# Kernel tuning notes

Hardware: AMD Instinct MI355X
Metric: run time of the kernel (lower is better)

## Reference

```python
import jax, jax.numpy as jnp
import numpy as np

# Module hyperparameters (match torch init_kwargs)
D_MODEL = 512
N_HEADS = 8
WINDOW_LEN = 128
DIL_FACTOR = 64
N_DIL = 2
ATTN_SINK = True
SRC_LEN = 2048
BSZ = 2


def setup_inputs() -> dict:
    key = jax.random.key(0)
    ks = jax.random.split(key, 6)
    w_scale = 0.04  # ~ xavier_uniform scale for 512x512
    inp = {
        "x": jax.random.normal(ks[0], (SRC_LEN, BSZ, D_MODEL), jnp.float32),
        "Wq": jax.random.normal(ks[1], (D_MODEL, D_MODEL), jnp.float32) * w_scale,
        "bq": jnp.zeros((D_MODEL,), jnp.float32),
        "Wk": jax.random.normal(ks[2], (D_MODEL, D_MODEL), jnp.float32) * w_scale,
        "bk": jnp.zeros((D_MODEL,), jnp.float32),
        "Wv": jax.random.normal(ks[3], (D_MODEL, D_MODEL), jnp.float32) * w_scale,
        "bv": jnp.zeros((D_MODEL,), jnp.float32),
        "Wo": jax.random.normal(ks[4], (D_MODEL, D_MODEL), jnp.float32) * w_scale,
        "bo": jnp.zeros((D_MODEL,), jnp.float32),
        "beta": jnp.zeros((N_HEADS,), jnp.float32),
    }
    return inp


def _fast_attention(x, Wq, bq, Wk, bk, Wv, bv, Wo, bo, beta):
    s, b, dm = x.shape  # (src_len, bsz, d_model)
    h = N_HEADS
    d = dm // h
    q = x @ Wq.T + bq
    k = x @ Wk.T + bk
    v = x @ Wv.T + bv

    def split_heads(t):  # 's b (h d) -> (b h) s d'
        return t.reshape(s, b, h, d).transpose(1, 2, 0, 3).reshape(b * h, s, d)

    q, k, v = split_heads(q), split_heads(k), split_heads(v)

    # beta: per-head temperature, tiled over batch (matches torch .repeat(bsz,1,1))
    beta_e = jnp.tile(jnp.exp(beta), b)[:, None, None]  # (b*h, 1, 1)
    q = q / (jnp.sqrt(jnp.asarray(d, q.dtype)) * beta_e)

    attn_out = jnp.zeros_like(v)
    z = b * h
    for i in range(N_DIL):
        dil = DIL_FACTOR ** i
        p = (WINDOW_LEN - 1) * dil
        pad = (p % s) if (p % s) != p else 0  # static python ints
        nw = pad // dil + 1  # num windows
        # causal left-padded strided windowed view of q: (z, nw, s, d)
        qp = jnp.pad(q, ((0, 0), (pad, 0), (0, 0)))
        idx = (jnp.arange(nw) * dil)[:, None] + jnp.arange(s)[None, :]  # (nw, s)
        qi = qp[:, idx, :]
        w = jnp.einsum('zbsd,zsd->zbs', qi, k)  # (z, nw, s)
        if ATTN_SINK:
            w = jnp.concatenate([w, jnp.zeros((z, 1, s), w.dtype)], axis=1)
        w = jax.nn.softmax(w, axis=1)  # softmax over window axis (+ sink)
        if ATTN_SINK:
            w = w[:, :-1]
        k2 = jnp.einsum('zbs,zsd->zbd', w, k)  # (z, nw, d)
        v2 = jnp.einsum('zbs,zsd->zbd', w, v)
        # left-pad back to full length (zeros at front, values at end)
        k = jnp.pad(k2, ((0, 0), (s - nw, 0), (0, 0)))
        v = jnp.pad(v2, ((0, 0), (s - nw, 0), (0, 0)))
        attn_out = attn_out + v

    # '(b h) s d -> s b (h d)'
    out = attn_out.reshape(b, h, s, d).transpose(2, 0, 1, 3).reshape(s, b, dm)
    return out @ Wo.T + bo


def reference(x, Wq, bq, Wk, bk, Wv, bv, Wo, bo, beta):
    return _fast_attention(x, Wq, bq, Wk, bk, Wv, bv, Wo, bo, beta)
```

## Files before the change

kernel.cpp:

```cpp
#include <hip/hip_runtime.h>
#include <math.h>

#define S_LEN 2048
#define BSZ 2
#define DM 512
#define NH 8
#define HD 64
#define RTOT (S_LEN*BSZ)
#define T_KEEP 32
#define ROW0 ((S_LEN - T_KEEP)*BSZ)

typedef __attribute__((ext_vector_type(8))) _Float16 half8;
typedef __attribute__((ext_vector_type(4))) float floatx4;

__device__ __forceinline__ half8 pack8(float4 a, float4 b) {
    half8 h;
    h[0]=(_Float16)a.x; h[1]=(_Float16)a.y; h[2]=(_Float16)a.z; h[3]=(_Float16)a.w;
    h[4]=(_Float16)b.x; h[5]=(_Float16)b.y; h[6]=(_Float16)b.z; h[7]=(_Float16)b.w;
    return h;
}

__global__ __launch_bounds__(256, 1) void mega(
    const float* __restrict__ x,
    const float* __restrict__ Wq, const float* __restrict__ Wk,
    const float* __restrict__ bq, const float* __restrict__ bk,
    const float* __restrict__ beta, const float* __restrict__ bo,
    float* __restrict__ spart, float* __restrict__ ssump,
    float* __restrict__ qsel, float* __restrict__ out)
{
    __shared__ __align__(16) char smem[65536];

    const int tid  = threadIdx.x;
    const int w    = tid >> 6;
    const int lane = tid & 63;
    const int lrow = lane & 15;
    const int lk8  = lane >> 4;
    const int bid  = blockIdx.x;
    const int rc   = (bid & 7)*4 + (bid >> 6);
    const int h    = (bid >> 3) & 7;
    const int r0   = rc * 128;

    {
        const float4* b4 = (const float4*)bo;
        float4* o4 = (float4*)out + (size_t)bid*2016;
        const int base = bid*2016;
        #pragma unroll
        for (int i = 0; i < 8; ++i) {
            int idx = i*256 + tid;
            if (idx < 2016) o4[idx] = b4[(base + idx) & 127];
        }
    }

    const int jsub = lk8;
    const int l15  = lrow;

    #pragma unroll
    for (int i = 0; i < 8; ++i) {
        const int chunk = w*8 + i;
        const int j = chunk*4 + jsub;
        const int s = l15 ^ (j & 15);
        const float* src = (j < 64 ? Wq + (size_t)(h*HD + j)*DM
                                   : Wk + (size_t)(h*HD + j - 64)*DM) + s*8;
        float4 f0 = *(const float4*)src;
        float4 f1 = *(const float4*)(src + 4);
        *(half8*)(smem + chunk*1024 + jsub*256 + l15*16) = pack8(f0, f1);
    }

    const float* xA = x + (size_t)(r0 + w*16 + lrow)*DM + lk8*8;
    const float* xB = x + (size_t)(r0 + (w+4)*16 + lrow)*DM + lk8*8;

    half8 Aa[4], Ab[4];
    #pragma unroll
    for (int kc2 = 0; kc2 < 4; ++kc2) {
        Aa[kc2] = pack8(*(const float4*)(xA + kc2*32), *(const float4*)(xA + kc2*32 + 4));
        Ab[kc2] = pack8(*(const float4*)(xB + kc2*32), *(const float4*)(xB + kc2*32 + 4));
    }

    floatx4 acc[2][8];
    #pragma unroll
    for (int jt = 0; jt < 8; ++jt) { acc[0][jt] = (floatx4)0.f; acc[1][jt] = (floatx4)0.f; }

    __syncthreads();

    #pragma unroll
    for (int kq = 0; kq < 4; ++kq) {
        const char* buf = smem + (kq & 1)*32768;
        char* nb = smem + ((kq + 1) & 1)*32768;

        float4 WF0[8], WF1[8];
        if (kq < 3) {
            #pragma unroll
            for (int i = 0; i < 8; ++i) {
                const int j = (w*8 + i)*4 + jsub;
                const int s = l15 ^ (j & 15);
                const float* src = (j < 64 ? Wq + (size_t)(h*HD + j)*DM
                                           : Wk + (size_t)(h*HD + j - 64)*DM)
                                   + (kq+1)*128 + s*8;
                WF0[i] = *(const float4*)src;
                WF1[i] = *(const float4*)(src + 4);
            }
        }

        #pragma unroll
        for (int kc2 = 0; kc2 < 4; ++kc2) {
            #pragma unroll
            for (int jt = 0; jt < 8; ++jt) {
                const int j = jt*16 + lrow;
                const int slotp = (kc2*4 + lk8) ^ lrow;
                half8 bf = *(const half8*)(buf + j*256 + slotp*16);
                acc[0][jt] = __builtin_amdgcn_mfma_f32_16x16x32_f16(Aa[kc2], bf, acc[0][jt], 0, 0, 0);
                acc[1][jt] = __builtin_amdgcn_mfma_f32_16x16x32_f16(Ab[kc2], bf, acc[1][jt], 0, 0, 0);
            }
            if (kq < 3) {
                Aa[kc2] = pack8(*(const float4*)(xA + (kq+1)*128 + kc2*32),
                                *(const float4*)(xA + (kq+1)*128 + kc2*32 + 4));
                Ab[kc2] = pack8(*(const float4*)(xB + (kq+1)*128 + kc2*32),
                                *(const float4*)(xB + (kq+1)*128 + kc2*32 + 4));
            }
        }

        if (kq < 3) {
            #pragma unroll
            for (int i = 0; i < 8; ++i)
                *(half8*)(nb + (w*8 + i)*1024 + jsub*256 + l15*16) = pack8(WF0[i], WF1[i]);
        }
        __syncthreads();
    }

    float* s_sig = (float*)smem;
    float bqv[4], bkv[4];
    #pragma unroll
    for (int jt = 0; jt < 4; ++jt) {
        bqv[jt] = bq[h*HD + jt*16 + lrow];
        bkv[jt] = bk[h*HD + jt*16 + lrow];
    }
    const float isc = 1.0f / (8.0f * expf(beta[h]));

    #pragma unroll
    for (int t = 0; t < 2; ++t) {
        #pragma unroll
        for (int r = 0; r < 4; ++r) {
            float q[4]; float p = 0.f;
            #pragma unroll
            for (int jt = 0; jt < 4; ++jt) {
                float qv = acc[t][jt][r]   + bqv[jt];
                float kv = acc[t][jt+4][r] + bkv[jt];
                q[jt] = qv;
                p += qv * kv;
            }
            p += __shfl_xor(p, 1, 64);
            p += __shfl_xor(p, 2, 64);
            p += __shfl_xor(p, 4, 64);
            p += __shfl_xor(p, 8, 64);
            const int rowl = (w + t*4)*16 + lk8*4 + r;
            if (lrow == 0)
                s_sig[rowl] = 1.0f / (1.0f + expf(-p * isc));
            if (rowl >= 126) {
                const int b = rowl & 1;
                float* qd = &qsel[((size_t)((b*NH + h)*T_KEEP) + rc)*64];
                #pragma unroll
                for (int jt = 0; jt < 4; ++jt) qd[jt*16 + lrow] = q[jt];
            }
        }
    }
    __syncthreads();

    {
        const int b  = tid & 1;
        const int cg = tid >> 1;
        const float* px = x + (size_t)(r0 + b)*DM + cg*4;
        float a0=0.f, a1=0.f, a2=0.f, a3=0.f;
        #pragma unroll 16
        for (int si = 0; si < 64; ++si) {
            const float sg = s_sig[si*2 + b];
            const float4 xv = *(const float4*)(px + (size_t)(si*2)*DM);
            a0 += sg*xv.x; a1 += sg*xv.y; a2 += sg*xv.z; a3 += sg*xv.w;
        }
        float4 st; st.x = a0; st.y = a1; st.z = a2; st.w = a3;
        *(float4*)&spart[((size_t)(rc*2 + b)*8 + h)*512 + cg*4] = st;
    }
    if (tid < 2) {
        float s = 0.f;
        for (int i = 0; i < 64; ++i) s += s_sig[i*2 + tid];
        ssump[(rc*2 + tid)*8 + h] = s;
    }
}

__global__ __launch_bounds__(256) void kvc(
    const float* __restrict__ spart, const float* __restrict__ ssump,
    const float* __restrict__ qsel, const float* __restrict__ beta,
    const float* __restrict__ Wk, const float* __restrict__ bk,
    const float* __restrict__ Wv, const float* __restrict__ bv,
    float* __restrict__ vbar, float* __restrict__ coef)
{
    const int z  = blockIdx.x >> 1;
    const int kv = blockIdx.x & 1;
    const int b  = z >> 3;
    const int h  = z & 7;
    const int tid = threadIdx.x;

    __shared__ float s_sb[DM];
    __shared__ float s_red[64][4];
    __shared__ float s_kb[64];
    __shared__ float s_part[T_KEEP][8];
    __shared__ float s_S;

    {
        const float2* sp = (const float2*)spart;
        float ax = 0.f, ay = 0.f;
        #pragma unroll
        for (int rcc = 0; rcc < 32; ++rcc) {
            float2 v = sp[((size_t)(rcc*2 + b)*8 + h)*256 + tid];
            ax += v.x; ay += v.y;
        }
        s_sb[tid*2] = ax; s_sb[tid*2+1] = ay;
    }
    {
        float sv = 0.f;
        if (tid < 32) sv = ssump[(tid*2 + b)*8 + h];
        if (tid < 64) {
            sv += __shfl_xor(sv, 1, 64);
            sv += __shfl_xor(sv, 2, 64);
            sv += __shfl_xor(sv, 4, 64);
            sv += __shfl_xor(sv, 8, 64);
            sv += __shfl_xor(sv, 16, 64);
            if (tid == 0) s_S = sv;
        }
    }
    __syncthreads();
    const float S = s_S;

    const float* W    = kv ? Wv : Wk;
    const float* bvec = kv ? bv : bk;
    {
        const int j = tid >> 2, kp = tid & 3;
        const float* wr = &W[(size_t)(h*HD + j)*DM + kp*128];
        float a = 0.f;
        #pragma unroll
        for (int k = 0; k < 128; k += 4) {
            float4 w4 = *(const float4*)&wr[k];
            int k0 = kp*128 + k;
            a += w4.x*s_sb[k0] + w4.y*s_sb[k0+1] + w4.z*s_sb[k0+2] + w4.w*s_sb[k0+3];
        }
        s_red[j][kp] = a;
    }
    __syncthreads();
    if (tid < 64) {
        float val = s_red[tid][0]+s_red[tid][1]+s_red[tid][2]+s_red[tid][3]
                  + bvec[h*HD + tid]*S;
        if (kv) vbar[z*HD + tid] = val;
        else    s_kb[tid] = val;
    }
    if (kv) return;
    __syncthreads();
    {
        const int wi = tid >> 3, jg = tid & 7;
        const float* qrow = &qsel[((size_t)z*T_KEEP + wi)*64 + jg*8];
        float4 q1 = *(const float4*)qrow;
        float4 q2 = *(const float4*)(qrow + 4);
        const int j0 = jg*8;
        float p = q1.x*s_kb[j0]   + q1.y*s_kb[j0+1] + q1.z*s_kb[j0+2] + q1.w*s_kb[j0+3]
                + q2.x*s_kb[j0+4] + q2.y*s_kb[j0+5] + q2.z*s_kb[j0+6] + q2.w*s_kb[j0+7];
        s_part[wi][jg] = p;
    }
    __syncthreads();
    if (tid < T_KEEP) {
        float sc = 0.f;
        #pragma unroll
        for (int gg = 0; gg < 8; ++gg) sc += s_part[tid][gg];
        sc *= 1.0f / (8.0f * expf(beta[h]));
        float m = sc;
        #pragma unroll
        for (int off = 16; off > 0; off >>= 1) m = fmaxf(m, __shfl_xor(m, off, 64));
        m = fmaxf(m, 0.f);
        float e = expf(sc - m);
        float d = e;
        #pragma unroll
        for (int off = 16; off > 0; off >>= 1) d += __shfl_xor(d, off, 64);
        d += expf(-m);
        float c = e / d;
        if (tid == T_KEEP-1) c += 1.0f;
        coef[z*T_KEEP + tid] = c;
    }
}

__global__ __launch_bounds__(256) void gout(
    const float* __restrict__ coef, const float* __restrict__ vbar,
    const float* __restrict__ Wo, const float* __restrict__ bo,
    float* __restrict__ out)
{
    const int b  = blockIdx.x & 1;
    const int cc = blockIdx.x >> 1;
    const int tid = threadIdx.x;

    __shared__ float s_cf[NH][T_KEEP];
    __shared__ float s_vb[NH*HD];
    __shared__ float s_gp[16][NH][2];

    s_vb[tid]       = vbar[b*512 + tid];
    s_vb[tid + 256] = vbar[b*512 + 256 + tid];
    s_cf[tid >> 5][tid & 31] = coef[((size_t)(b*NH) + (tid >> 5))*T_KEEP + (tid & 31)];
    __syncthreads();

    {
        const int ci = tid & 15, hh = (tid >> 4) & 7, j2 = tid >> 7;
        const float* wr = &Wo[(size_t)(cc*16 + ci)*DM + hh*HD + j2*32];
        const float* vb = &s_vb[hh*HD + j2*32];
        float a = 0.f;
        #pragma unroll
        for (int j = 0; j < 32; j += 4) {
            float4 w4 = *(const float4*)&wr[j];
            a += w4.x*vb[j] + w4.y*vb[j+1] + w4.z*vb[j+2] + w4.w*vb[j+3];
        }
        s_gp[ci][hh][j2] = a;
    }
    __syncthreads();
    {
        const int ci = tid & 15;
        const float bov = bo[cc*16 + ci];
        #pragma unroll
        for (int hf = 0; hf < 2; ++hf) {
            const int wi = (tid >> 4) + hf*16;
            float v = bov;
            #pragma unroll
            for (int hh = 0; hh < NH; ++hh)
                v += s_cf[hh][wi] * (s_gp[ci][hh][0] + s_gp[ci][hh][1]);
            out[(size_t)(ROW0 + wi*2 + b)*DM + cc*16 + ci] = v;
        }
    }
}

extern "C" void kernel_launch(void* const* d_in, const int* in_sizes, int n_in,
                              void* d_out, int out_size, void* d_ws, size_t ws_size,
                              hipStream_t stream) {
    const float* x    = (const float*)d_in[0];
    const float* Wq   = (const float*)d_in[1];
    const float* bq   = (const float*)d_in[2];
    const float* Wk   = (const float*)d_in[3];
    const float* bk   = (const float*)d_in[4];
    const float* Wv   = (const float*)d_in[5];
    const float* bv   = (const float*)d_in[6];
    const float* Wo   = (const float*)d_in[7];
    const float* bo   = (const float*)d_in[8];
    const float* beta = (const float*)d_in[9];

    char* ws = (char*)d_ws;
    float* spart = (float*)(ws + 0);
    float* ssump = (float*)(ws + 1048576);
    float* qsel  = (float*)(ws + 1052672);
    float* vbar  = (float*)(ws + 1183744);
    float* coef  = (float*)(ws + 1187840);
    float* out   = (float*)d_out;

    mega<<<256, 256, 0, stream>>>(x, Wq, Wk, bq, bk, beta, bo,
                                  spart, ssump, qsel, out);
    kvc<<<32, 256, 0, stream>>>(spart, ssump, qsel, beta,
                                Wk, bk, Wv, bv, vbar, coef);
    gout<<<64, 256, 0, stream>>>(coef, vbar, Wo, bo, out);
}
```

Before: 112.1 us.

## Fuse three kernels into one cooperative launch with grid syncs

Turns the three stage kernels into device functions and runs them inside a single cooperative kernel of 256 blocks, with grid-wide syncs between stages in place of kernel boundaries. This removes two kernel launch gaps. In exchange it adds grid barrier cost, and the later stages leave most blocks idle. If the cooperative launch fails, the code falls back to the original three launches.

```diff
diff --git a/kernel.cpp b/kernel.cpp
--- a/kernel.cpp
+++ b/kernel.cpp
@@ -1,5 +1,8 @@
 #include <hip/hip_runtime.h>
+#include <hip/hip_cooperative_groups.h>
 #include <math.h>
+
+namespace cg = cooperative_groups;
 
 #define S_LEN 2048
 #define BSZ 2
@@ -20,22 +23,20 @@
     return h;
 }
 
-__global__ __launch_bounds__(256, 1) void mega(
+
+__device__ void mega_body(
     const float* __restrict__ x,
     const float* __restrict__ Wq, const float* __restrict__ Wk,
     const float* __restrict__ bq, const float* __restrict__ bk,
     const float* __restrict__ beta, const float* __restrict__ bo,
     float* __restrict__ spart, float* __restrict__ ssump,
-    float* __restrict__ qsel, float* __restrict__ out)
-{
-    __shared__ __align__(16) char smem[65536];
-
-    const int tid  = threadIdx.x;
+    float* __restrict__ qsel, float* __restrict__ out,
+    char* smem, int bid, int tid)
+{
     const int w    = tid >> 6;
     const int lane = tid & 63;
     const int lrow = lane & 15;
     const int lk8  = lane >> 4;
-    const int bid  = blockIdx.x;
     const int rc   = (bid & 7)*4 + (bid >> 6);
     const int h    = (bid >> 3) & 7;
     const int r0   = rc * 128;
@@ -167,8 +168,8 @@
 
     {
         const int b  = tid & 1;
-        const int cg = tid >> 1;
-        const float* px = x + (size_t)(r0 + b)*DM + cg*4;
+        const int cg2 = tid >> 1;
+        const float* px = x + (size_t)(r0 + b)*DM + cg2*4;
         float a0=0.f, a1=0.f, a2=0.f, a3=0.f;
         #pragma unroll 16
         for (int si = 0; si < 64; ++si) {
@@ -177,7 +178,7 @@
             a0 += sg*xv.x; a1 += sg*xv.y; a2 += sg*xv.z; a3 += sg*xv.w;
         }
         float4 st; st.x = a0; st.y = a1; st.z = a2; st.w = a3;
-        *(float4*)&spart[((size_t)(rc*2 + b)*8 + h)*512 + cg*4] = st;
+        *(float4*)&spart[((size_t)(rc*2 + b)*8 + h)*512 + cg2*4] = st;
     }
     if (tid < 2) {
         float s = 0.f;
@@ -186,24 +187,24 @@
     }
 }
 
-__global__ __launch_bounds__(256) void kvc(
+__device__ void kvc_body(
     const float* __restrict__ spart, const float* __restrict__ ssump,
     const float* __restrict__ qsel, const float* __restrict__ beta,
     const float* __restrict__ Wk, const float* __restrict__ bk,
     const float* __restrict__ Wv, const float* __restrict__ bv,
-    float* __restrict__ vbar, float* __restrict__ coef)
-{
-    const int z  = blockIdx.x >> 1;
-    const int kv = blockIdx.x & 1;
+    float* __restrict__ vbar, float* __restrict__ coef,
+    char* smem, int bid, int tid)
+{
+    const int z  = bid >> 1;
+    const int kvv = bid & 1;
     const int b  = z >> 3;
     const int h  = z & 7;
-    const int tid = threadIdx.x;
-
-    __shared__ float s_sb[DM];
-    __shared__ float s_red[64][4];
-    __shared__ float s_kb[64];
-    __shared__ float s_part[T_KEEP][8];
-    __shared__ float s_S;
+
+    float* s_sb = (float*)smem;
+    float (*s_red)[4] = (float(*)[4])(smem + 2048);
+    float* s_kb = (float*)(smem + 3072);
+    float (*s_part)[8] = (float(*)[8])(smem + 3584);
+    float* s_S = (float*)(smem + 4608);
 
     {
         const float2* sp = (const float2*)spart;
@@ -224,14 +225,14 @@
             sv += __shfl_xor(sv, 4, 64);
             sv += __shfl_xor(sv, 8, 64);
             sv += __shfl_xor(sv, 16, 64);
-            if (tid == 0) s_S = sv;
-        }
-    }
-    __syncthreads();
-    const float S = s_S;
-
-    const float* W    = kv ? Wv : Wk;
-    const float* bvec = kv ? bv : bk;
+            if (tid == 0) *s_S = sv;
+        }
+    }
+    __syncthreads();
+    const float S = *s_S;
+
+    const float* W    = kvv ? Wv : Wk;
+    const float* bvec = kvv ? bv : bk;
     {
         const int j = tid >> 2, kp = tid & 3;
         const float* wr = &W[(size_t)(h*HD + j)*DM + kp*128];
@@ -248,54 +249,54 @@
     if (tid < 64) {
         float val = s_red[tid][0]+s_red[tid][1]+s_red[tid][2]+s_red[tid][3]
                   + bvec[h*HD + tid]*S;
-        if (kv) vbar[z*HD + tid] = val;
-        else    s_kb[tid] = val;
-    }
-    if (kv) return;
-    __syncthreads();
-    {
-        const int wi = tid >> 3, jg = tid & 7;
-        const float* qrow = &qsel[((size_t)z*T_KEEP + wi)*64 + jg*8];
-        float4 q1 = *(const float4*)qrow;
-        float4 q2 = *(const float4*)(qrow + 4);
-        const int j0 = jg*8;
-        float p = q1.x*s_kb[j0]   + q1.y*s_kb[j0+1] + q1.z*s_kb[j0+2] + q1.w*s_kb[j0+3]
-                + q2.x*s_kb[j0+4] + q2.y*s_kb[j0+5] + q2.z*s_kb[j0+6] + q2.w*s_kb[j0+7];
-        s_part[wi][jg] = p;
-    }
-    __syncthreads();
-    if (tid < T_KEEP) {
-        float sc = 0.f;
-        #pragma unroll
-        for (int gg = 0; gg < 8; ++gg) sc += s_part[tid][gg];
-        sc *= 1.0f / (8.0f * expf(beta[h]));
-        float m = sc;
-        #pragma unroll
-        for (int off = 16; off > 0; off >>= 1) m = fmaxf(m, __shfl_xor(m, off, 64));
-        m = fmaxf(m, 0.f);
-        float e = expf(sc - m);
-        float d = e;
-        #pragma unroll
-        for (int off = 16; off > 0; off >>= 1) d += __shfl_xor(d, off, 64);
-        d += expf(-m);
-        float c = e / d;
-        if (tid == T_KEEP-1) c += 1.0f;
-        coef[z*T_KEEP + tid] = c;
-    }
-}
-
-__global__ __launch_bounds__(256) void gout(
+        if (kvv) vbar[z*HD + tid] = val;
+        else     s_kb[tid] = val;
+    }
+    if (!kvv) {
+        __syncthreads();
+        {
+            const int wi = tid >> 3, jg = tid & 7;
+            const float* qrow = &qsel[((size_t)z*T_KEEP + wi)*64 + jg*8];
+            float4 q1 = *(const float4*)qrow;
+            float4 q2 = *(const float4*)(qrow + 4);
+            const int j0 = jg*8;
+            float p = q1.x*s_kb[j0]   + q1.y*s_kb[j0+1] + q1.z*s_kb[j0+2] + q1.w*s_kb[j0+3]
+                    + q2.x*s_kb[j0+4] + q2.y*s_kb[j0+5] + q2.z*s_kb[j0+6] + q2.w*s_kb[j0+7];
+            s_part[wi][jg] = p;
+        }
+        __syncthreads();
+        if (tid < T_KEEP) {
+            float sc = 0.f;
+            #pragma unroll
+            for (int gg = 0; gg < 8; ++gg) sc += s_part[tid][gg];
+            sc *= 1.0f / (8.0f * expf(beta[h]));
+            float m = sc;
+            #pragma unroll
+            for (int off = 16; off > 0; off >>= 1) m = fmaxf(m, __shfl_xor(m, off, 64));
+            m = fmaxf(m, 0.f);
+            float e = expf(sc - m);
+            float d = e;
+            #pragma unroll
+            for (int off = 16; off > 0; off >>= 1) d += __shfl_xor(d, off, 64);
+            d += expf(-m);
+            float c = e / d;
+            if (tid == T_KEEP-1) c += 1.0f;
+            coef[z*T_KEEP + tid] = c;
+        }
+    }
+}
+
+__device__ void gout_body(
     const float* __restrict__ coef, const float* __restrict__ vbar,
     const float* __restrict__ Wo, const float* __restrict__ bo,
-    float* __restrict__ out)
-{
-    const int b  = blockIdx.x & 1;
-    const int cc = blockIdx.x >> 1;
-    const int tid = threadIdx.x;
-
-    __shared__ float s_cf[NH][T_KEEP];
-    __shared__ float s_vb[NH*HD];
-    __shared__ float s_gp[16][NH][2];
+    float* __restrict__ out, char* smem, int bid, int tid)
+{
+    const int b  = bid & 1;
+    const int cc = bid >> 1;
+
+    float (*s_cf)[T_KEEP] = (float(*)[T_KEEP])smem;
+    float* s_vb = (float*)(smem + 1024);
+    float (*s_gp)[NH][2] = (float(*)[NH][2])(smem + 3072);
 
     s_vb[tid]       = vbar[b*512 + tid];
     s_vb[tid + 256] = vbar[b*512 + 256 + tid];
@@ -328,6 +329,70 @@
             out[(size_t)(ROW0 + wi*2 + b)*DM + cc*16 + ci] = v;
         }
     }
+}
+
+__global__ __launch_bounds__(256, 1) void fused(
+    const float* __restrict__ x,
+    const float* __restrict__ Wq, const float* __restrict__ Wk,
+    const float* __restrict__ Wv, const float* __restrict__ Wo,
+    const float* __restrict__ bq, const float* __restrict__ bk,
+    const float* __restrict__ bv, const float* __restrict__ bo,
+    const float* __restrict__ beta,
+    float* __restrict__ spart, float* __restrict__ ssump,
+    float* __restrict__ qsel, float* __restrict__ vbar,
+    float* __restrict__ coef, float* __restrict__ out)
+{
+    __shared__ __align__(16) char smem[65536];
+    const int bid = blockIdx.x;
+    const int tid = threadIdx.x;
+
+    mega_body(x, Wq, Wk, bq, bk, beta, bo, spart, ssump, qsel, out, smem, bid, tid);
+
+    __threadfence();
+    cg::this_grid().sync();
+
+    if (bid < 32)
+        kvc_body(spart, ssump, qsel, beta, Wk, bk, Wv, bv, vbar, coef, smem, bid, tid);
+
+    __threadfence();
+    cg::this_grid().sync();
+
+    if (bid < 64)
+        gout_body(coef, vbar, Wo, bo, out, smem, bid, tid);
+}
+
+__global__ __launch_bounds__(256, 1) void megaK(
+    const float* __restrict__ x,
+    const float* __restrict__ Wq, const float* __restrict__ Wk,
+    const float* __restrict__ bq, const float* __restrict__ bk,
+    const float* __restrict__ beta, const float* __restrict__ bo,
+    float* __restrict__ spart, float* __restrict__ ssump,
+    float* __restrict__ qsel, float* __restrict__ out)
+{
+    __shared__ __align__(16) char smem[65536];
+    mega_body(x, Wq, Wk, bq, bk, beta, bo, spart, ssump, qsel, out,
+              smem, blockIdx.x, threadIdx.x);
+}
+
+__global__ __launch_bounds__(256) void kvcK(
+    const float* __restrict__ spart, const float* __restrict__ ssump,
+    const float* __restrict__ qsel, const float* __restrict__ beta,
+    const float* __restrict__ Wk, const float* __restrict__ bk,
+    const float* __restrict__ Wv, const float* __restrict__ bv,
+    float* __restrict__ vbar, float* __restrict__ coef)
+{
+    __shared__ __align__(16) char smem[8192];
+    kvc_body(spart, ssump, qsel, beta, Wk, bk, Wv, bv, vbar, coef,
+             smem, blockIdx.x, threadIdx.x);
+}
+
+__global__ __launch_bounds__(256) void goutK(
+    const float* __restrict__ coef, const float* __restrict__ vbar,
+    const float* __restrict__ Wo, const float* __restrict__ bo,
+    float* __restrict__ out)
+{
+    __shared__ __align__(16) char smem[8192];
+    gout_body(coef, vbar, Wo, bo, out, smem, blockIdx.x, threadIdx.x);
 }
 
 extern "C" void kernel_launch(void* const* d_in, const int* in_sizes, int n_in,
@@ -352,9 +417,19 @@
     float* coef  = (float*)(ws + 1187840);
     float* out   = (float*)d_out;
 
-    mega<<<256, 256, 0, stream>>>(x, Wq, Wk, bq, bk, beta, bo,
-                                  spart, ssump, qsel, out);
-    kvc<<<32, 256, 0, stream>>>(spart, ssump, qsel, beta,
-                                Wk, bk, Wv, bv, vbar, coef);
-    gout<<<64, 256, 0, stream>>>(coef, vbar, Wo, bo, out);
-}
+    void* kargs[] = {
+        (void*)&x, (void*)&Wq, (void*)&Wk, (void*)&Wv, (void*)&Wo,
+        (void*)&bq, (void*)&bk, (void*)&bv, (void*)&bo, (void*)&beta,
+        (void*)&spart, (void*)&ssump, (void*)&qsel, (void*)&vbar,
+        (void*)&coef, (void*)&out
+    };
+    hipError_t err = hipLaunchCooperativeKernel(
+        reinterpret_cast<void*>(fused), dim3(256), dim3(256), kargs, 0, stream);
+    if (err != hipSuccess) {
+        megaK<<<256, 256, 0, stream>>>(x, Wq, Wk, bq, bk, beta, bo,
+                                       spart, ssump, qsel, out);
+        kvcK<<<32, 256, 0, stream>>>(spart, ssump, qsel, beta,
+                                     Wk, bk, Wv, bv, vbar, coef);
+        goutK<<<64, 256, 0, stream>>>(coef, vbar, Wo, bo, out);
+    }
+}
```

Result: slower. 263.2 us (+134.8%).

## Fuse kvc and gout into one tail kernel with atomic output accumulation

Applied to the files above, without the earlier changes.

Merges the K/V reduction kernel and the output-projection kernel into a single 16-block kernel. Each block computes kbar and vbar for its head, the window coefficients, and the per-head Wo projection, then atomically adds its contribution into the last 32 output rows. The mega kernel now writes the bias into every output row, so the atomics accumulate on top of it. This removes one launch and the workspace round trip. In exchange it relies on 16 blocks doing many float atomics, which gives low parallelism and a nondeterministic summation order.

```diff
diff --git a/kernel.cpp b/kernel.cpp
--- a/kernel.cpp
+++ b/kernel.cpp
@@ -42,12 +42,12 @@
 
     {
         const float4* b4 = (const float4*)bo;
-        float4* o4 = (float4*)out + (size_t)bid*2016;
-        const int base = bid*2016;
+        float4* o4 = (float4*)out + (size_t)bid*2048;
+        const int base = bid*2048;
         #pragma unroll
         for (int i = 0; i < 8; ++i) {
             int idx = i*256 + tid;
-            if (idx < 2016) o4[idx] = b4[(base + idx) & 127];
+            o4[idx] = b4[(base + idx) & 127];
         }
     }
 
@@ -186,23 +186,23 @@
     }
 }
 
-__global__ __launch_bounds__(256) void kvc(
+__global__ __launch_bounds__(256) void tailk(
     const float* __restrict__ spart, const float* __restrict__ ssump,
     const float* __restrict__ qsel, const float* __restrict__ beta,
     const float* __restrict__ Wk, const float* __restrict__ bk,
     const float* __restrict__ Wv, const float* __restrict__ bv,
-    float* __restrict__ vbar, float* __restrict__ coef)
+    const float* __restrict__ Wo, float* __restrict__ out)
 {
-    const int z  = blockIdx.x >> 1;
-    const int kv = blockIdx.x & 1;
-    const int b  = z >> 3;
-    const int h  = z & 7;
+    const int z = blockIdx.x;
+    const int b = z >> 3;
+    const int h = z & 7;
     const int tid = threadIdx.x;
 
     __shared__ float s_sb[DM];
-    __shared__ float s_red[64][4];
-    __shared__ float s_kb[64];
+    __shared__ float s_red2[128][2];
+    __shared__ float s_kb[64], s_vb[64];
     __shared__ float s_part[T_KEEP][8];
+    __shared__ float s_cf[T_KEEP];
     __shared__ float s_S;
 
     {
@@ -230,29 +230,32 @@
     __syncthreads();
     const float S = s_S;
 
-    const float* W    = kv ? Wv : Wk;
-    const float* bvec = kv ? bv : bk;
-    {
-        const int j = tid >> 2, kp = tid & 3;
-        const float* wr = &W[(size_t)(h*HD + j)*DM + kp*128];
+    {
+        const int idx  = tid >> 1;
+        const int kp   = tid & 1;
+        const int j    = idx & 63;
+        const int kind = idx >> 6;
+        const float* W = kind ? Wv : Wk;
+        const float* wr = &W[(size_t)(h*HD + j)*DM + kp*256];
+        const float* sb = &s_sb[kp*256];
         float a = 0.f;
         #pragma unroll
-        for (int k = 0; k < 128; k += 4) {
+        for (int k = 0; k < 256; k += 4) {
             float4 w4 = *(const float4*)&wr[k];
-            int k0 = kp*128 + k;
-            a += w4.x*s_sb[k0] + w4.y*s_sb[k0+1] + w4.z*s_sb[k0+2] + w4.w*s_sb[k0+3];
-        }
-        s_red[j][kp] = a;
-    }
-    __syncthreads();
-    if (tid < 64) {
-        float val = s_red[tid][0]+s_red[tid][1]+s_red[tid][2]+s_red[tid][3]
-                  + bvec[h*HD + tid]*S;
-        if (kv) vbar[z*HD + tid] = val;
-        else    s_kb[tid] = val;
-    }
-    if (kv) return;
-    __syncthreads();
+            a += w4.x*sb[k] + w4.y*sb[k+1] + w4.z*sb[k+2] + w4.w*sb[k+3];
+        }
+        s_red2[idx][kp] = a;
+    }
+    __syncthreads();
+    if (tid < 128) {
+        const int j = tid & 63, kind = tid >> 6;
+        float val = s_red2[tid][0] + s_red2[tid][1]
+                  + (kind ? bv : bk)[h*HD + j]*S;
+        if (kind) s_vb[j] = val;
+        else      s_kb[j] = val;
+    }
+    __syncthreads();
+
     {
         const int wi = tid >> 3, jg = tid & 7;
         const float* qrow = &qsel[((size_t)z*T_KEEP + wi)*64 + jg*8];
@@ -280,53 +283,23 @@
         d += expf(-m);
         float c = e / d;
         if (tid == T_KEEP-1) c += 1.0f;
-        coef[z*T_KEEP + tid] = c;
-    }
-}
-
-__global__ __launch_bounds__(256) void gout(
-    const float* __restrict__ coef, const float* __restrict__ vbar,
-    const float* __restrict__ Wo, const float* __restrict__ bo,
-    float* __restrict__ out)
-{
-    const int b  = blockIdx.x & 1;
-    const int cc = blockIdx.x >> 1;
-    const int tid = threadIdx.x;
-
-    __shared__ float s_cf[NH][T_KEEP];
-    __shared__ float s_vb[NH*HD];
-    __shared__ float s_gp[16][NH][2];
-
-    s_vb[tid]       = vbar[b*512 + tid];
-    s_vb[tid + 256] = vbar[b*512 + 256 + tid];
-    s_cf[tid >> 5][tid & 31] = coef[((size_t)(b*NH) + (tid >> 5))*T_KEEP + (tid & 31)];
-    __syncthreads();
-
-    {
-        const int ci = tid & 15, hh = (tid >> 4) & 7, j2 = tid >> 7;
-        const float* wr = &Wo[(size_t)(cc*16 + ci)*DM + hh*HD + j2*32];
-        const float* vb = &s_vb[hh*HD + j2*32];
-        float a = 0.f;
-        #pragma unroll
-        for (int j = 0; j < 32; j += 4) {
+        s_cf[tid] = c;
+    }
+    __syncthreads();
+
+    #pragma unroll
+    for (int cc2 = 0; cc2 < 2; ++cc2) {
+        const int c = cc2*256 + tid;
+        const float* wr = &Wo[(size_t)c*DM + h*HD];
+        float g = 0.f;
+        #pragma unroll
+        for (int j = 0; j < 64; j += 4) {
             float4 w4 = *(const float4*)&wr[j];
-            a += w4.x*vb[j] + w4.y*vb[j+1] + w4.z*vb[j+2] + w4.w*vb[j+3];
-        }
-        s_gp[ci][hh][j2] = a;
-    }
-    __syncthreads();
-    {
-        const int ci = tid & 15;
-        const float bov = bo[cc*16 + ci];
-        #pragma unroll
-        for (int hf = 0; hf < 2; ++hf) {
-            const int wi = (tid >> 4) + hf*16;
-            float v = bov;
-            #pragma unroll
-            for (int hh = 0; hh < NH; ++hh)
-                v += s_cf[hh][wi] * (s_gp[ci][hh][0] + s_gp[ci][hh][1]);
-            out[(size_t)(ROW0 + wi*2 + b)*DM + cc*16 + ci] = v;
-        }
+            g += w4.x*s_vb[j] + w4.y*s_vb[j+1] + w4.z*s_vb[j+2] + w4.w*s_vb[j+3];
+        }
+        #pragma unroll
+        for (int wi = 0; wi < T_KEEP; ++wi)
+            atomicAdd(&out[(size_t)(ROW0 + wi*2 + b)*DM + c], s_cf[wi]*g);
     }
 }
 
@@ -348,13 +321,10 @@
     float* spart = (float*)(ws + 0);
     float* ssump = (float*)(ws + 1048576);
     float* qsel  = (float*)(ws + 1052672);
-    float* vbar  = (float*)(ws + 1183744);
-    float* coef  = (float*)(ws + 1187840);
     float* out   = (float*)d_out;
 
     mega<<<256, 256, 0, stream>>>(x, Wq, Wk, bq, bk, beta, bo,
                                   spart, ssump, qsel, out);
-    kvc<<<32, 256, 0, stream>>>(spart, ssump, qsel, beta,
-                                Wk, bk, Wv, bv, vbar, coef);
-    gout<<<64, 256, 0, stream>>>(coef, vbar, Wo, bo, out);
+    tailk<<<16, 256, 0, stream>>>(spart, ssump, qsel, beta,
+                                  Wk, bk, Wv, bv, Wo, out);
 }
```

New measurement: 118.5 us. 5.7% more time.
